# Performance work log

Measured on AMD Instinct MI355X. Metric: run time of the kernel, lower is better.

The kernel has to match this reference:

```python
import jax, jax.numpy as jnp
import numpy as np

B, T, C = 4, 2048, 1024
H, D = 16, 64

def setup_inputs() -> dict:
    key = jax.random.key(0)
    k1, k2, k3 = jax.random.split(key, 3)
    x = jax.random.normal(k1, (B, T, C), dtype=jnp.float32)
    Wqkv = jax.random.normal(k2, (C, 3 * C), dtype=jnp.float32) * (1.0 / np.sqrt(C))
    Wproj = jax.random.normal(k3, (C, C), dtype=jnp.float32) * (1.0 / np.sqrt(C))
    return {"x": x, "Wqkv": Wqkv, "Wproj": Wproj}

def reference(x, Wqkv, Wproj):
    Bx, Tx, Cx = x.shape
    qkv = x @ Wqkv                       # (B, T, 3C)
    q, k, v = jnp.split(qkv, 3, axis=-1)
    # (B, T, C) -> (B, H, T, D)
    q = q.reshape(Bx, Tx, H, D).transpose(0, 2, 1, 3)
    k = k.reshape(Bx, Tx, H, D).transpose(0, 2, 1, 3)
    v = v.reshape(Bx, Tx, H, D).transpose(0, 2, 1, 3)
    att = jnp.einsum('bhqd,bhkd->bhqk', q, k) / jnp.sqrt(jnp.float32(D))
    causal = jnp.tril(jnp.ones((Tx, Tx), dtype=bool))  # (T, T)
    att = jnp.where(causal[None, None, :, :], att, jnp.float32(-jnp.inf))
    att = jax.nn.softmax(att, axis=-1)
    y = jnp.einsum('bhqk,bhkd->bhqd', att, v)          # (B, H, T, D)
    y = y.transpose(0, 2, 1, 3).reshape(Bx, Tx, Cx)
    return y @ Wproj
```

## Files before the change

kernel.cpp:

```cpp
#include <hip/hip_runtime.h>
#include <cstdint>
#include <cstddef>


typedef short bf16x8 __attribute__((ext_vector_type(8)));
typedef float f32x4 __attribute__((ext_vector_type(4)));

#define MFMA32(a, b, c) __builtin_amdgcn_mfma_f32_16x16x32_bf16((a), (b), (c), 0, 0, 0)

__device__ __forceinline__ unsigned short f2b(float f) {
  unsigned int x = __builtin_bit_cast(unsigned int, f);
  x += 0x7fffu + ((x >> 16) & 1u);
  return (unsigned short)(x >> 16);
}

__device__ __forceinline__ unsigned int pack2(float a, float b) {
  return (unsigned int)f2b(a) | ((unsigned int)f2b(b) << 16);
}

__device__ __forceinline__ unsigned int cvtpk(float a, float b) {
  unsigned int r;
  asm("v_cvt_pk_bf16_f32 %0, %1, %2" : "=v"(r) : "v"(a), "v"(b));
  return r;
}

__device__ __forceinline__ float exp2v(float x) {
  float r;
  asm("v_exp_f32 %0, %1" : "=v"(r) : "v"(x));
  return r;
}

__device__ __forceinline__ void gload16(const void* g, void* l) {
  __builtin_amdgcn_global_load_lds(
      (const __attribute__((address_space(1))) void*)g,
      (__attribute__((address_space(3))) void*)l, 16, 0, 0);
}

__global__ __launch_bounds__(256) void k_conv_x(const float* __restrict__ in,
                                                unsigned short* __restrict__ out, int n4) {
  int i = blockIdx.x * 256 + threadIdx.x;
  if (i >= n4) return;
  float4 v = reinterpret_cast<const float4*>(in)[i];
  ushort4 o;
  o.x = f2b(v.x); o.y = f2b(v.y); o.z = f2b(v.z); o.w = f2b(v.w);
  reinterpret_cast<ushort4*>(out)[i] = o;
}

__global__ __launch_bounds__(256) void k_transpose(const float* __restrict__ in,
                                                   unsigned short* __restrict__ out,
                                                   int R, int C) {
  __shared__ float tile[32][33];
  int c0 = blockIdx.x * 32, r0 = blockIdx.y * 32;
  int tx = threadIdx.x & 31, ty = threadIdx.x >> 5;
#pragma unroll
  for (int j = 0; j < 4; ++j)
    tile[ty + 8 * j][tx] = in[(size_t)(r0 + ty + 8 * j) * C + c0 + tx];
  __syncthreads();
#pragma unroll
  for (int j = 0; j < 4; ++j)
    out[(size_t)(c0 + ty + 8 * j) * R + r0 + tx] = f2b(tile[tx][ty + 8 * j]);
}

template <int EPI>
__global__ __launch_bounds__(256) void k_gemm(const unsigned short* __restrict__ A,
                                              const unsigned short* __restrict__ Bt,
                                              float* __restrict__ outF,
                                              unsigned short* __restrict__ q_ws,
                                              unsigned short* __restrict__ k_ws,
                                              unsigned short* __restrict__ v_ws,
                                              int M, int N) {
  constexpr int K = 1024;
  __shared__ unsigned short smem[16384];
  unsigned short* As = smem;
  unsigned short* Bs = smem + 8192;
  const int bn = blockIdx.x, bm = blockIdx.y;
  const int tid = threadIdx.x;
  const int w = tid >> 6, lane = tid & 63;
  const int wm = w >> 1, wn = w & 1;
  const int c = lane & 15, g = lane >> 4;
  const int cl8 = c & 7;

  f32x4 acc[4][4];
#pragma unroll
  for (int i = 0; i < 4; ++i)
#pragma unroll
    for (int j = 0; j < 4; ++j) acc[i][j] = (f32x4){0.f, 0.f, 0.f, 0.f};

  const int srow = 32 * w + (lane >> 3);
  const int scol = 8 * ((lane & 7) ^ (lane >> 3));
  const unsigned short* Ag = A + (size_t)(bm * 128 + srow) * K + scol;
  const unsigned short* Bg = Bt + (size_t)(bn * 128 + srow) * K + scol;
  char* AsB = (char*)As + w * 4096;
  char* BsB = (char*)Bs + w * 4096;

  for (int kt = 0; kt < K / 64; ++kt) {
    const int kb = kt * 64;
    __syncthreads();
#pragma unroll
    for (int i = 0; i < 4; ++i) {
      gload16(Ag + (size_t)(8 * i) * K + kb, AsB + i * 1024);
      gload16(Bg + (size_t)(8 * i) * K + kb, BsB + i * 1024);
    }
    asm volatile("s_waitcnt vmcnt(0)" ::: "memory");
    __syncthreads();
#pragma unroll
    for (int u = 0; u < 2; ++u) {
      bf16x8 af[4], bfr[4];
#pragma unroll
      for (int mf = 0; mf < 4; ++mf)
        af[mf] = *(const bf16x8*)((const char*)As + (wm * 64 + mf * 16 + c) * 128 +
                                  (((u * 4 + g) ^ cl8) * 16));
#pragma unroll
      for (int nf = 0; nf < 4; ++nf)
        bfr[nf] = *(const bf16x8*)((const char*)Bs + (wn * 64 + nf * 16 + c) * 128 +
                                   (((u * 4 + g) ^ cl8) * 16));
#pragma unroll
      for (int mf = 0; mf < 4; ++mf)
#pragma unroll
        for (int nf = 0; nf < 4; ++nf)
          acc[mf][nf] = MFMA32(af[mf], bfr[nf], acc[mf][nf]);
    }
  }

  const int rowb = bm * 128 + wm * 64;
  const int colb = bn * 128 + wn * 64;
  if (EPI == 1) {
#pragma unroll
    for (int mf = 0; mf < 4; ++mf)
#pragma unroll
      for (int nf = 0; nf < 4; ++nf)
#pragma unroll
        for (int r = 0; r < 4; ++r) {
          int row = rowb + mf * 16 + 4 * g + r;
          int col = colb + nf * 16 + c;
          outF[(size_t)row * N + col] = acc[mf][nf][r];
        }
  } else {
    const int sec = colb >> 10;
    const int hh = (colb & 1023) >> 6;
    const int b = rowb >> 11, t0 = rowb & 2047;
    unsigned short* Lw = smem + w * 4096;

    __syncthreads();
    if (sec < 2) {
      const float sc = (sec == 0) ? 0.125f * 1.4426950408889634f : 1.f;
#pragma unroll
      for (int mf = 0; mf < 4; ++mf)
#pragma unroll
        for (int nf = 0; nf < 4; ++nf)
#pragma unroll
          for (int r = 0; r < 4; ++r)
            Lw[(16 * mf + 4 * g + r) * 64 + 16 * nf + c] = f2b(acc[mf][nf][r] * sc);
    } else {
#pragma unroll
      for (int mf = 0; mf < 4; ++mf)
#pragma unroll
        for (int nf = 0; nf < 4; ++nf)
#pragma unroll
          for (int rr = 0; rr < 2; ++rr)
            *(unsigned int*)&Lw[(16 * nf + c) * 64 + 16 * mf + 4 * g + 2 * rr] =
                pack2(acc[mf][nf][2 * rr], acc[mf][nf][2 * rr + 1]);
    }
    asm volatile("s_waitcnt lgkmcnt(0)" ::: "memory");
    const int rw = lane >> 3, ch = lane & 7;
    const int chx = ch ^ rw;
    if (sec == 0) {
      unsigned short* dst = q_ws + ((size_t)(b * 16 + hh) * 2048 + t0) * 64;
#pragma unroll
      for (int i = 0; i < 8; ++i) {
        int tl = i * 8 + rw;
        *(bf16x8*)(dst + (size_t)tl * 64 + ch * 8) = *(const bf16x8*)&Lw[tl * 64 + ch * 8];
      }
    } else if (sec == 1) {
      unsigned short* dst = k_ws + ((size_t)(b * 16 + hh) * 2048 + t0) * 64;
#pragma unroll
      for (int i = 0; i < 8; ++i) {
        int tl = i * 8 + rw;
        *(bf16x8*)(dst + (size_t)tl * 64 + chx * 8) = *(const bf16x8*)&Lw[tl * 64 + ch * 8];
      }
    } else {
      unsigned short* dst = v_ws + (size_t)(b * 16 + hh) * 64 * 2048 + t0;
#pragma unroll
      for (int i = 0; i < 8; ++i) {
        int dl = i * 8 + rw;
        *(bf16x8*)(dst + (size_t)dl * 2048 + chx * 8) = *(const bf16x8*)&Lw[dl * 64 + ch * 8];
      }
    }
  }
}

__global__ __launch_bounds__(512) void k_attn(const unsigned short* __restrict__ q_ws,
                                              const unsigned short* __restrict__ k_ws,
                                              const unsigned short* __restrict__ v_ws,
                                              unsigned short* __restrict__ y_ws) {
  constexpr int T = 2048;
  __shared__ unsigned short Ks[2][64 * 64];
  __shared__ unsigned short Vs[2][64 * 64];
  const int f = blockIdx.x;
  const int f2 = (f & 7) * 64 + (f >> 3);
  const int bh = f2 >> 3;
  const int xi = f2 & 7;
  const int tid = threadIdx.x, w = tid >> 6, lane = tid & 63;
  const int c = lane & 15, g = lane >> 4;
  const int cl = c & 7;
  const size_t base = (size_t)bh * T * 64;
  const unsigned short* Kb = k_ws + base;
  const unsigned short* Vb = v_ws + base;
  const unsigned short* Qb = q_ws + base;

  const int srow = w * 8 + (lane >> 3);
  const int sch = lane & 7;

#pragma unroll 1
  for (int ph = 0; ph < 2; ++ph) {
    const int q0 = (ph == 0 ? xi : 15 - xi) * 128;
    const int qrow = q0 + 16 * w + c;
    const int q_max_wave = q0 + 16 * w + 15;
    const int n_kt = (q0 >> 6) + 2;
    bf16x8 qf[2];
#pragma unroll
    for (int u = 0; u < 2; ++u)
      qf[u] = *(const bf16x8*)(Qb + (size_t)qrow * 64 + 32 * u + 8 * g);

    f32x4 yacc[4];
#pragma unroll
    for (int i = 0; i < 4; ++i) yacc[i] = (f32x4){0.f, 0.f, 0.f, 0.f};
    float m_run = -1e30f, l_part = 0.f;

    __syncthreads();
    gload16(Kb + (size_t)srow * 64 + sch * 8, (char*)&Ks[0][0] + w * 1024);
    gload16(Vb + (size_t)srow * T + sch * 8, (char*)&Vs[0][0] + w * 1024);

#pragma unroll 1
    for (int kt = 0; kt < n_kt; ++kt) {
      const int k0 = kt * 64;
      const int cur = kt & 1;
      if (kt + 1 < n_kt) {
        const int k0n = k0 + 64;
        gload16(Kb + (size_t)(k0n + srow) * 64 + sch * 8, (char*)&Ks[cur ^ 1][0] + w * 1024);
        gload16(Vb + (size_t)srow * T + k0n + sch * 8, (char*)&Vs[cur ^ 1][0] + w * 1024);
        asm volatile("s_waitcnt vmcnt(2)" ::: "memory");
      } else {
        asm volatile("s_waitcnt vmcnt(0)" ::: "memory");
      }
      __builtin_amdgcn_s_barrier();

      if (k0 <= q_max_wave) {
        const char* KsC = (const char*)&Ks[cur][0];
        const char* VsC = (const char*)&Vs[cur][0];
        f32x4 s[4];
        __builtin_amdgcn_s_setprio(1);
#pragma unroll
        for (int tf = 0; tf < 4; ++tf) {
          bf16x8 kf0 = *(const bf16x8*)(KsC + (16 * tf + c) * 128 + (g ^ cl) * 16);
          bf16x8 kf1 = *(const bf16x8*)(KsC + (16 * tf + c) * 128 + ((4 + g) ^ cl) * 16);
          f32x4 z = (f32x4){0.f, 0.f, 0.f, 0.f};
          z = MFMA32(kf0, qf[0], z);
          s[tf] = MFMA32(kf1, qf[1], z);
        }
        __builtin_amdgcn_s_setprio(0);
        if (k0 + 63 > q0 + 16 * w) {
#pragma unroll
          for (int tf = 0; tf < 4; ++tf)
#pragma unroll
            for (int r = 0; r < 4; ++r)
              if (k0 + 16 * tf + 4 * g + r > qrow) s[tf][r] = -1e30f;
        }
        float mx0 = fmaxf(fmaxf(s[0][0], s[0][1]), fmaxf(s[0][2], s[0][3]));
        float mx1 = fmaxf(fmaxf(s[1][0], s[1][1]), fmaxf(s[1][2], s[1][3]));
        float mx2 = fmaxf(fmaxf(s[2][0], s[2][1]), fmaxf(s[2][2], s[2][3]));
        float mx3 = fmaxf(fmaxf(s[3][0], s[3][1]), fmaxf(s[3][2], s[3][3]));
        float mx = fmaxf(fmaxf(mx0, mx1), fmaxf(mx2, mx3));
        mx = fmaxf(mx, __shfl_xor(mx, 16));
        mx = fmaxf(mx, __shfl_xor(mx, 32));
        if (__any(mx > m_run + 11.5f)) {
          float m_new = fmaxf(m_run, mx);
          float corr = exp2v(m_run - m_new);
          l_part *= corr;
#pragma unroll
          for (int i = 0; i < 4; ++i) yacc[i] *= corr;
          m_run = m_new;
        }
        float p[16];
#pragma unroll
        for (int tf = 0; tf < 4; ++tf)
#pragma unroll
          for (int r = 0; r < 4; ++r) p[tf * 4 + r] = exp2v(s[tf][r] - m_run);
        float ps = ((p[0] + p[1]) + (p[2] + p[3])) + ((p[4] + p[5]) + (p[6] + p[7]));
        ps += ((p[8] + p[9]) + (p[10] + p[11])) + ((p[12] + p[13]) + (p[14] + p[15]));
        l_part += ps;

#pragma unroll
        for (int h = 0; h < 2; ++h) {
          unsigned int lo0 = cvtpk(p[8 * h + 0], p[8 * h + 1]);
          unsigned int hi0 = cvtpk(p[8 * h + 2], p[8 * h + 3]);
          unsigned int lo1 = cvtpk(p[8 * h + 4], p[8 * h + 5]);
          unsigned int hi1 = cvtpk(p[8 * h + 6], p[8 * h + 7]);
          int a2 = 2 * (g & 1);
          int srcA = 16 * a2 + c, srcB = srcA + 16;
          unsigned int Al0 = __shfl(lo0, srcA), Ah0 = __shfl(hi0, srcA);
          unsigned int Al1 = __shfl(lo1, srcA), Ah1 = __shfl(hi1, srcA);
          unsigned int Bl0 = __shfl(lo0, srcB), Bh0 = __shfl(hi0, srcB);
          unsigned int Bl1 = __shfl(lo1, srcB), Bh1 = __shfl(hi1, srcB);
          bool f1 = (g >= 2);
          union { unsigned int u[4]; bf16x8 v; } pf;
          pf.u[0] = f1 ? Al1 : Al0;
          pf.u[1] = f1 ? Ah1 : Ah0;
          pf.u[2] = f1 ? Bl1 : Bl0;
          pf.u[3] = f1 ? Bh1 : Bh0;
          __builtin_amdgcn_s_setprio(1);
#pragma unroll
          for (int df = 0; df < 4; ++df) {
            bf16x8 vf = *(const bf16x8*)(VsC + (16 * df + c) * 128 + ((h * 4 + g) ^ cl) * 16);
            yacc[df] = MFMA32(vf, pf.v, yacc[df]);
          }
          __builtin_amdgcn_s_setprio(0);
        }
      }
      __builtin_amdgcn_s_barrier();
    }

    float lt = l_part;
    lt += __shfl_xor(lt, 16);
    lt += __shfl_xor(lt, 32);
    float inv = 1.f / lt;
    const int b = bh >> 4, hh = bh & 15;
#pragma unroll
    for (int df = 0; df < 4; ++df) {
      uint2 o;
      o.x = cvtpk(yacc[df][0] * inv, yacc[df][1] * inv);
      o.y = cvtpk(yacc[df][2] * inv, yacc[df][3] * inv);
      *(uint2*)(y_ws + (size_t)(b * 2048 + qrow) * 1024 + hh * 64 + 16 * df + 4 * g) = o;
    }
  }
}

extern "C" void kernel_launch(void* const* d_in, const int* in_sizes, int n_in,
                              void* d_out, int out_size, void* d_ws, size_t ws_size,
                              hipStream_t stream) {
  const float* x = (const float*)d_in[0];
  const float* Wqkv = (const float*)d_in[1];
  const float* Wproj = (const float*)d_in[2];
  float* out = (float*)d_out;
  char* ws = (char*)d_ws;

  unsigned short* x_bf = (unsigned short*)(ws);
  unsigned short* wqkvT = (unsigned short*)(ws + 16777216);
  unsigned short* wprojT = (unsigned short*)(ws + 23068672);
  unsigned short* q_ws = (unsigned short*)(ws + 25165824);
  unsigned short* k_ws = (unsigned short*)(ws + 41943040);
  unsigned short* v_ws = (unsigned short*)(ws + 58720256);
  unsigned short* y_ws = (unsigned short*)(ws + 75497472);

  k_conv_x<<<8192, 256, 0, stream>>>(x, x_bf, 2097152);
  k_transpose<<<dim3(96, 32), 256, 0, stream>>>(Wqkv, wqkvT, 1024, 3072);
  k_transpose<<<dim3(32, 32), 256, 0, stream>>>(Wproj, wprojT, 1024, 1024);
  k_gemm<0><<<dim3(24, 64), 256, 0, stream>>>(x_bf, wqkvT, nullptr, q_ws, k_ws, v_ws, 8192, 3072);
  k_attn<<<512, 512, 0, stream>>>(q_ws, k_ws, v_ws, y_ws);
  k_gemm<1><<<dim3(8, 64), 256, 0, stream>>>(y_ws, wprojT, out, nullptr, nullptr, nullptr, 8192, 1024);
}
```

Measured before the change: 186.4 us.

## Switch attention kernel to 32x32x16 MFMA with 4 waves of 32 query rows

Rewrites the attention inner loop to use 32x32x16 bf16 MFMA instead of 16x16x32. Each wave now owns 32 query rows, so the block has 4 waves (256 threads) instead of 8, and each thread issues two K/V tile loads per stage. The P-matrix repacking needs only a single xor-32 shuffle instead of many cross-lane shuffles, and row-max and row-sum reductions need fewer shuffles. The cost is larger accumulator register use and fewer waves per block, which may reduce latency hiding. Causal skipping also becomes coarser at 32-row granularity.

```diff
diff --git a/kernel.cpp b/kernel.cpp
--- a/kernel.cpp
+++ b/kernel.cpp
@@ -5,8 +5,10 @@
 
 typedef short bf16x8 __attribute__((ext_vector_type(8)));
 typedef float f32x4 __attribute__((ext_vector_type(4)));
+typedef float f32x16 __attribute__((ext_vector_type(16)));
 
 #define MFMA32(a, b, c) __builtin_amdgcn_mfma_f32_16x16x32_bf16((a), (b), (c), 0, 0, 0)
+#define MFMA3216(a, b, c) __builtin_amdgcn_mfma_f32_32x32x16_bf16((a), (b), (c), 0, 0, 0)
 
 __device__ __forceinline__ unsigned short f2b(float f) {
   unsigned int x = __builtin_bit_cast(unsigned int, f);
@@ -189,10 +191,10 @@
   }
 }
 
-__global__ __launch_bounds__(512) void k_attn(const unsigned short* __restrict__ q_ws,
-                                              const unsigned short* __restrict__ k_ws,
-                                              const unsigned short* __restrict__ v_ws,
-                                              unsigned short* __restrict__ y_ws) {
+__global__ __launch_bounds__(256, 4) void k_attn(const unsigned short* __restrict__ q_ws,
+                                                 const unsigned short* __restrict__ k_ws,
+                                                 const unsigned short* __restrict__ v_ws,
+                                                 unsigned short* __restrict__ y_ws) {
   constexpr int T = 2048;
   __shared__ unsigned short Ks[2][64 * 64];
   __shared__ unsigned short Vs[2][64 * 64];
@@ -201,35 +203,40 @@
   const int bh = f2 >> 3;
   const int xi = f2 & 7;
   const int tid = threadIdx.x, w = tid >> 6, lane = tid & 63;
-  const int c = lane & 15, g = lane >> 4;
-  const int cl = c & 7;
+  const int q32 = lane & 31;
+  const int hi = lane >> 5;
+  const int l7 = lane & 7;
   const size_t base = (size_t)bh * T * 64;
   const unsigned short* Kb = k_ws + base;
   const unsigned short* Vb = v_ws + base;
   const unsigned short* Qb = q_ws + base;
 
-  const int srow = w * 8 + (lane >> 3);
+  const int srow = w * 16 + (lane >> 3);
   const int sch = lane & 7;
 
 #pragma unroll 1
   for (int ph = 0; ph < 2; ++ph) {
     const int q0 = (ph == 0 ? xi : 15 - xi) * 128;
-    const int qrow = q0 + 16 * w + c;
-    const int q_max_wave = q0 + 16 * w + 15;
+    const int qb = q0 + 32 * w;
+    const int qcol = qb + q32;
     const int n_kt = (q0 >> 6) + 2;
-    bf16x8 qf[2];
-#pragma unroll
-    for (int u = 0; u < 2; ++u)
-      qf[u] = *(const bf16x8*)(Qb + (size_t)qrow * 64 + 32 * u + 8 * g);
-
-    f32x4 yacc[4];
-#pragma unroll
-    for (int i = 0; i < 4; ++i) yacc[i] = (f32x4){0.f, 0.f, 0.f, 0.f};
+    bf16x8 qf[4];
+#pragma unroll
+    for (int ks = 0; ks < 4; ++ks)
+      qf[ks] = *(const bf16x8*)(Qb + (size_t)qcol * 64 + 16 * ks + 8 * hi);
+
+    f32x16 yacc[2];
+#pragma unroll
+    for (int db = 0; db < 2; ++db)
+#pragma unroll
+      for (int i = 0; i < 16; ++i) yacc[db][i] = 0.f;
     float m_run = -1e30f, l_part = 0.f;
 
     __syncthreads();
-    gload16(Kb + (size_t)srow * 64 + sch * 8, (char*)&Ks[0][0] + w * 1024);
-    gload16(Vb + (size_t)srow * T + sch * 8, (char*)&Vs[0][0] + w * 1024);
+    gload16(Kb + (size_t)srow * 64 + sch * 8, (char*)&Ks[0][0] + w * 2048);
+    gload16(Kb + (size_t)(srow + 8) * 64 + sch * 8, (char*)&Ks[0][0] + w * 2048 + 1024);
+    gload16(Vb + (size_t)srow * T + sch * 8, (char*)&Vs[0][0] + w * 2048);
+    gload16(Vb + (size_t)(srow + 8) * T + sch * 8, (char*)&Vs[0][0] + w * 2048 + 1024);
 
 #pragma unroll 1
     for (int kt = 0; kt < n_kt; ++kt) {
@@ -237,82 +244,99 @@
       const int cur = kt & 1;
       if (kt + 1 < n_kt) {
         const int k0n = k0 + 64;
-        gload16(Kb + (size_t)(k0n + srow) * 64 + sch * 8, (char*)&Ks[cur ^ 1][0] + w * 1024);
-        gload16(Vb + (size_t)srow * T + k0n + sch * 8, (char*)&Vs[cur ^ 1][0] + w * 1024);
-        asm volatile("s_waitcnt vmcnt(2)" ::: "memory");
+        char* KsW = (char*)&Ks[cur ^ 1][0] + w * 2048;
+        char* VsW = (char*)&Vs[cur ^ 1][0] + w * 2048;
+        gload16(Kb + (size_t)(k0n + srow) * 64 + sch * 8, KsW);
+        gload16(Kb + (size_t)(k0n + srow + 8) * 64 + sch * 8, KsW + 1024);
+        gload16(Vb + (size_t)srow * T + k0n + sch * 8, VsW);
+        gload16(Vb + (size_t)(srow + 8) * T + k0n + sch * 8, VsW + 1024);
+        asm volatile("s_waitcnt vmcnt(4)" ::: "memory");
       } else {
         asm volatile("s_waitcnt vmcnt(0)" ::: "memory");
       }
       __builtin_amdgcn_s_barrier();
 
-      if (k0 <= q_max_wave) {
+      if (k0 <= qb + 31) {
         const char* KsC = (const char*)&Ks[cur][0];
         const char* VsC = (const char*)&Vs[cur][0];
-        f32x4 s[4];
+        f32x16 s[2];
+#pragma unroll
+        for (int tb = 0; tb < 2; ++tb)
+#pragma unroll
+          for (int i = 0; i < 16; ++i) s[tb][i] = 0.f;
         __builtin_amdgcn_s_setprio(1);
 #pragma unroll
-        for (int tf = 0; tf < 4; ++tf) {
-          bf16x8 kf0 = *(const bf16x8*)(KsC + (16 * tf + c) * 128 + (g ^ cl) * 16);
-          bf16x8 kf1 = *(const bf16x8*)(KsC + (16 * tf + c) * 128 + ((4 + g) ^ cl) * 16);
-          f32x4 z = (f32x4){0.f, 0.f, 0.f, 0.f};
-          z = MFMA32(kf0, qf[0], z);
-          s[tf] = MFMA32(kf1, qf[1], z);
+        for (int ks = 0; ks < 4; ++ks) {
+          const int chk = ((2 * ks + hi) ^ l7) * 16;
+#pragma unroll
+          for (int tb = 0; tb < 2; ++tb) {
+            const int row = 32 * tb + q32;
+            bf16x8 kf = *(const bf16x8*)(KsC + row * 128 + chk);
+            s[tb] = MFMA3216(kf, qf[ks], s[tb]);
+          }
         }
         __builtin_amdgcn_s_setprio(0);
-        if (k0 + 63 > q0 + 16 * w) {
-#pragma unroll
-          for (int tf = 0; tf < 4; ++tf)
-#pragma unroll
-            for (int r = 0; r < 4; ++r)
-              if (k0 + 16 * tf + 4 * g + r > qrow) s[tf][r] = -1e30f;
-        }
-        float mx0 = fmaxf(fmaxf(s[0][0], s[0][1]), fmaxf(s[0][2], s[0][3]));
-        float mx1 = fmaxf(fmaxf(s[1][0], s[1][1]), fmaxf(s[1][2], s[1][3]));
-        float mx2 = fmaxf(fmaxf(s[2][0], s[2][1]), fmaxf(s[2][2], s[2][3]));
-        float mx3 = fmaxf(fmaxf(s[3][0], s[3][1]), fmaxf(s[3][2], s[3][3]));
-        float mx = fmaxf(fmaxf(mx0, mx1), fmaxf(mx2, mx3));
-        mx = fmaxf(mx, __shfl_xor(mx, 16));
+        if (k0 + 63 > qb) {
+#pragma unroll
+          for (int tb = 0; tb < 2; ++tb)
+#pragma unroll
+            for (int r = 0; r < 16; ++r) {
+              int tk = k0 + 32 * tb + (r & 3) + 8 * (r >> 2) + 4 * hi;
+              if (tk > qcol) s[tb][r] = -1e30f;
+            }
+        }
+        float mx = s[0][0];
+#pragma unroll
+        for (int tb = 0; tb < 2; ++tb)
+#pragma unroll
+          for (int r = 0; r < 16; ++r) mx = fmaxf(mx, s[tb][r]);
         mx = fmaxf(mx, __shfl_xor(mx, 32));
         if (__any(mx > m_run + 11.5f)) {
           float m_new = fmaxf(m_run, mx);
           float corr = exp2v(m_run - m_new);
           l_part *= corr;
 #pragma unroll
-          for (int i = 0; i < 4; ++i) yacc[i] *= corr;
+          for (int db = 0; db < 2; ++db)
+#pragma unroll
+            for (int i = 0; i < 16; ++i) yacc[db][i] *= corr;
           m_run = m_new;
         }
-        float p[16];
-#pragma unroll
-        for (int tf = 0; tf < 4; ++tf)
-#pragma unroll
-          for (int r = 0; r < 4; ++r) p[tf * 4 + r] = exp2v(s[tf][r] - m_run);
-        float ps = ((p[0] + p[1]) + (p[2] + p[3])) + ((p[4] + p[5]) + (p[6] + p[7]));
-        ps += ((p[8] + p[9]) + (p[10] + p[11])) + ((p[12] + p[13]) + (p[14] + p[15]));
+        unsigned pk[2][8];
+        float ps = 0.f;
+#pragma unroll
+        for (int tb = 0; tb < 2; ++tb)
+#pragma unroll
+          for (int q4 = 0; q4 < 4; ++q4) {
+            float p0 = exp2v(s[tb][4 * q4 + 0] - m_run);
+            float p1 = exp2v(s[tb][4 * q4 + 1] - m_run);
+            float p2 = exp2v(s[tb][4 * q4 + 2] - m_run);
+            float p3 = exp2v(s[tb][4 * q4 + 3] - m_run);
+            ps += ((p0 + p1) + (p2 + p3));
+            pk[tb][2 * q4] = cvtpk(p0, p1);
+            pk[tb][2 * q4 + 1] = cvtpk(p2, p3);
+          }
         l_part += ps;
 
 #pragma unroll
-        for (int h = 0; h < 2; ++h) {
-          unsigned int lo0 = cvtpk(p[8 * h + 0], p[8 * h + 1]);
-          unsigned int hi0 = cvtpk(p[8 * h + 2], p[8 * h + 3]);
-          unsigned int lo1 = cvtpk(p[8 * h + 4], p[8 * h + 5]);
-          unsigned int hi1 = cvtpk(p[8 * h + 6], p[8 * h + 7]);
-          int a2 = 2 * (g & 1);
-          int srcA = 16 * a2 + c, srcB = srcA + 16;
-          unsigned int Al0 = __shfl(lo0, srcA), Ah0 = __shfl(hi0, srcA);
-          unsigned int Al1 = __shfl(lo1, srcA), Ah1 = __shfl(hi1, srcA);
-          unsigned int Bl0 = __shfl(lo0, srcB), Bh0 = __shfl(hi0, srcB);
-          unsigned int Bl1 = __shfl(lo1, srcB), Bh1 = __shfl(hi1, srcB);
-          bool f1 = (g >= 2);
-          union { unsigned int u[4]; bf16x8 v; } pf;
-          pf.u[0] = f1 ? Al1 : Al0;
-          pf.u[1] = f1 ? Ah1 : Ah0;
-          pf.u[2] = f1 ? Bl1 : Bl0;
-          pf.u[3] = f1 ? Bh1 : Bh0;
+        for (int kw = 0; kw < 4; ++kw) {
+          const int tb = kw >> 1, a = kw & 1;
+          unsigned g00 = pk[tb][4 * a + 0], g01 = pk[tb][4 * a + 1];
+          unsigned g10 = pk[tb][4 * a + 2], g11 = pk[tb][4 * a + 3];
+          unsigned own0 = hi ? g10 : g00, own1 = hi ? g11 : g01;
+          unsigned snd0 = hi ? g00 : g10, snd1 = hi ? g01 : g11;
+          unsigned X0 = __shfl_xor(snd0, 32), X1 = __shfl_xor(snd1, 32);
+          union { unsigned int u[4]; bf16x8 v; } pb;
+          pb.u[0] = hi ? X0 : own0;
+          pb.u[1] = hi ? X1 : own1;
+          pb.u[2] = hi ? own0 : X0;
+          pb.u[3] = hi ? own1 : X1;
+          const int chv = ((2 * kw + hi) ^ l7) * 16;
           __builtin_amdgcn_s_setprio(1);
 #pragma unroll
-          for (int df = 0; df < 4; ++df) {
-            bf16x8 vf = *(const bf16x8*)(VsC + (16 * df + c) * 128 + ((h * 4 + g) ^ cl) * 16);
-            yacc[df] = MFMA32(vf, pf.v, yacc[df]);
+          for (int db = 0; db < 2; ++db) {
+            const int row = 32 * db + q32;
+            bf16x8 vf = *(const bf16x8*)(VsC + row * 128 + chv);
+            yacc[db] = MFMA3216(vf, pb.v, yacc[db]);
           }
           __builtin_amdgcn_s_setprio(0);
         }
@@ -320,18 +344,19 @@
       __builtin_amdgcn_s_barrier();
     }
 
-    float lt = l_part;
-    lt += __shfl_xor(lt, 16);
-    lt += __shfl_xor(lt, 32);
+    float lt = l_part + __shfl_xor(l_part, 32);
     float inv = 1.f / lt;
     const int b = bh >> 4, hh = bh & 15;
-#pragma unroll
-    for (int df = 0; df < 4; ++df) {
-      uint2 o;
-      o.x = cvtpk(yacc[df][0] * inv, yacc[df][1] * inv);
-      o.y = cvtpk(yacc[df][2] * inv, yacc[df][3] * inv);
-      *(uint2*)(y_ws + (size_t)(b * 2048 + qrow) * 1024 + hh * 64 + 16 * df + 4 * g) = o;
-    }
+    unsigned short* yrow = y_ws + (size_t)(b * 2048 + qcol) * 1024 + hh * 64;
+#pragma unroll
+    for (int db = 0; db < 2; ++db)
+#pragma unroll
+      for (int rg = 0; rg < 4; ++rg) {
+        uint2 o;
+        o.x = cvtpk(yacc[db][4 * rg + 0] * inv, yacc[db][4 * rg + 1] * inv);
+        o.y = cvtpk(yacc[db][4 * rg + 2] * inv, yacc[db][4 * rg + 3] * inv);
+        *(uint2*)(yrow + 32 * db + 8 * rg + 4 * hi) = o;
+      }
   }
 }
 
@@ -356,6 +381,6 @@
   k_transpose<<<dim3(96, 32), 256, 0, stream>>>(Wqkv, wqkvT, 1024, 3072);
   k_transpose<<<dim3(32, 32), 256, 0, stream>>>(Wproj, wprojT, 1024, 1024);
   k_gemm<0><<<dim3(24, 64), 256, 0, stream>>>(x_bf, wqkvT, nullptr, q_ws, k_ws, v_ws, 8192, 3072);
-  k_attn<<<512, 512, 0, stream>>>(q_ws, k_ws, v_ws, y_ws);
+  k_attn<<<512, 256, 0, stream>>>(q_ws, k_ws, v_ws, y_ws);
   k_gemm<1><<<dim3(8, 64), 256, 0, stream>>>(y_ws, wprojT, out, nullptr, nullptr, nullptr, 8192, 1024);
 }
```

Measured after the change: 183.4 us. No clear change (-1.6%).
